# Kernel tuning notes

Hardware: AMD Instinct MI355X
Metric: run time of the kernel (lower is better)

The kernel has to match this reference:

```python
import jax, jax.numpy as jnp
import numpy as np

D = 256      # feature_dim (d_model)
H = 4        # num_heads
N = 4096     # query nodes
M = 4096     # source nodes


def _conv1x1(W, b, x):
    # Conv1d(kernel_size=1): per-position linear over channels. x: [1, Cin, N]
    return jnp.einsum('oi,bin->bon', W, x) + b[None, :, None]


def setup_inputs() -> dict:
    key = jax.random.key(0)
    ks = jax.random.split(key, 16)
    s = 0.02
    inp = {
        'x':      jax.random.normal(ks[0], (1, D, N), jnp.float32),
        'source': jax.random.normal(ks[1], (1, D, M), jnp.float32),
        'dist':   jax.random.uniform(ks[2], (1, N, M), jnp.float32),
        'mask':   jax.random.bernoulli(ks[3], 0.5, (N, M)),
        'Wq': s * jax.random.normal(ks[4], (D, D), jnp.float32),  'bq': jnp.zeros((D,), jnp.float32),
        'Wk': s * jax.random.normal(ks[5], (D, D), jnp.float32),  'bk': jnp.zeros((D,), jnp.float32),
        'Wv': s * jax.random.normal(ks[6], (D, D), jnp.float32),  'bv': jnp.zeros((D,), jnp.float32),
        'Wm': s * jax.random.normal(ks[7], (D, D), jnp.float32),  'bm': jnp.zeros((D,), jnp.float32),
        'W1': s * jax.random.normal(ks[8], (2 * D, 2 * D), jnp.float32), 'b1': jnp.zeros((2 * D,), jnp.float32),
        'W2': s * jax.random.normal(ks[9], (D, 2 * D), jnp.float32),     'b2': jnp.zeros((D,), jnp.float32),
    }
    return inp


def reference(x, source, dist, mask, Wq, bq, Wk, bk, Wv, bv, Wm, bm, W1, b1, W2, b2):
    dim = D // H  # per-head dim; torch view(1, dim, H, -1) splits channels as (dim, H)
    q = _conv1x1(Wq, bq, x).reshape(1, dim, H, N)
    k = _conv1x1(Wk, bk, source).reshape(1, dim, H, M)
    v = _conv1x1(Wv, bv, source).reshape(1, dim, H, M)

    scores = jnp.einsum('bdhn,bdhm->bhnm', q, k) / jnp.sqrt(jnp.asarray(dim, q.dtype))
    # non-standard additive mask: global detached min scales the masked-out entries
    smin = jax.lax.stop_gradient(scores.min())
    scores = scores + smin * (~mask).astype(scores.dtype)[None, None, :, :]

    prob = jax.nn.softmax(scores, axis=-1)                       # [1,H,N,M]
    attn = jnp.einsum('bhnm,bdhm->bdhn', prob, v)                # [1,dim,H,N]
    message = _conv1x1(Wm, bm, attn.reshape(1, D, N))            # merge heads

    h = jnp.concatenate([x, message], axis=1)                    # [1,2D,N]
    h = jax.nn.relu(_conv1x1(W1, b1, h))
    y = _conv1x1(W2, b2, h)                                      # [1,D,N]
    weights = scores.mean(axis=1)                                # [1,N,M]
    return y, weights
```

## Files before the change

### kernel.cpp

```cpp
#include <hip/hip_runtime.h>
#include <hip/hip_bf16.h>
#include <math.h>

#define Dm 256
#define Hh 4
#define Nn 4096
#define Mq 4096

typedef __attribute__((ext_vector_type(8))) short bf16x8;
typedef __attribute__((ext_vector_type(4))) float f32x4;
typedef _Float16 __attribute__((ext_vector_type(4))) f16x4;
typedef __fp16 __attribute__((ext_vector_type(2))) h16x2;

#define MFMA_BF16(a,b,c) __builtin_amdgcn_mfma_f32_16x16x32_bf16(a,b,c,0,0,0)
#define MFMA_F16x16(a,b,c) __builtin_amdgcn_mfma_f32_16x16x16f16(a,b,c,0,0,0)

#define MB (1u<<20)
#define OFF_FLAG  0
#define OFF_SMIN  64
#define OFF_KMAX  128
#define OFF_PART  1024
#define OFF_MT    8192
#define OFF_DENP  (128u<<10)
#define OFF_WB    (3u*MB/2)
#define OFF_BITS  (3u*MB)
#define OFF_QB    (5u*MB)
#define OFF_KB    (7u*MB)
#define OFF_VB    (9u*MB)
#define OFF_HCAT  (11u*MB)
#define OFF_ATTNT (15u*MB)
#define OFF_XT    (17u*MB)
#define OFF_ST    (19u*MB)
#define OFF_OPART (17u*MB)
#define OFF_H1T   (17u*MB)

#define WOFF_Q  0
#define WOFF_K  65536
#define WOFF_V  131072
#define WOFF_M  196608
#define WOFF_1  262144
#define WOFF_2  524288

__device__ __forceinline__ unsigned short f2bf(float x) {
    unsigned u = __float_as_uint(x);
    u += 0x7FFF + ((u >> 16) & 1);
    return (unsigned short)(u >> 16);
}
__device__ __forceinline__ float bf2f(unsigned short b) {
    return __uint_as_float(((unsigned)b) << 16);
}

__global__ void k_detect(const unsigned char* __restrict__ mb, int* __restrict__ flag,
                         unsigned* __restrict__ kmax) {
    __shared__ int c[5];
    if (threadIdx.x < 5) c[threadIdx.x] = 0;
    if (threadIdx.x < 4) kmax[threadIdx.x] = 0u;
    __syncthreads();
    for (int i = threadIdx.x; i < 16384; i += blockDim.x) {
        unsigned char b = mb[i];
        if (b) {
            atomicAdd(&c[i & 3], 1);
            if ((i & 7) == 4) atomicAdd(&c[4], 1);
        }
    }
    __syncthreads();
    if (threadIdx.x == 0) {
        int f;
        if (c[3] > 0 && c[0] == 0)          f = 3;
        else if (c[1] | c[2] | c[3])        f = 1;
        else if (c[4] > 0)                  f = 0;
        else                                f = 2;
        *flag = f;
    }
}

__global__ void k_maskbits(const void* __restrict__ mp, const int* __restrict__ flagp,
                           unsigned char* __restrict__ bits) {
    size_t i = (size_t)blockIdx.x * 256 + threadIdx.x;
    const int flag = *flagp;
    size_t base = i * 8;
    unsigned b = 0;
    if (flag == 1) {
        unsigned long long u = *(const unsigned long long*)((const unsigned char*)mp + base);
        #pragma unroll
        for (int j = 0; j < 8; j++) b |= (unsigned)(((u >> (8*j)) & 0xFFull) != 0ull) << j;
    } else if (flag == 0) {
        const int* p = (const int*)mp;
        #pragma unroll
        for (int j = 0; j < 8; j++) b |= (unsigned)(p[base + j] != 0) << j;
    } else if (flag == 3) {
        const float* p = (const float*)mp;
        #pragma unroll
        for (int j = 0; j < 8; j++) b |= (unsigned)(p[base + j] != 0.0f) << j;
    } else {
        const unsigned long long* p = (const unsigned long long*)mp;
        #pragma unroll
        for (int j = 0; j < 8; j++) b |= (unsigned)(p[base + j] != 0ull) << j;
    }
    bits[i] = (unsigned char)b;
}

__global__ __launch_bounds__(256) void k_prep(const float* __restrict__ x,
                                              const float* __restrict__ source,
                                              unsigned short* __restrict__ xt,
                                              unsigned short* __restrict__ st,
                                              unsigned short* __restrict__ hcat) {
    const int z = blockIdx.z;
    const float* src = z ? source : x;
    unsigned short* dst = z ? st : xt;
    unsigned short* dst2 = z ? nullptr : hcat;
    const int l = threadIdx.x & 63, g = threadIdx.x >> 6;
    const int c = blockIdx.y * 64 + l;
    const int n0 = blockIdx.x * 32 + g * 8;
    float4 v0 = *(const float4*)(src + (size_t)c * Nn + n0);
    float4 v1 = *(const float4*)(src + (size_t)c * Nn + n0 + 4);
    float vv[8] = {v0.x, v0.y, v0.z, v0.w, v1.x, v1.y, v1.z, v1.w};
    #pragma unroll
    for (int j = 0; j < 8; j++) {
        unsigned short b = f2bf(vv[j]);
        dst[(size_t)(n0 + j) * 256 + c] = b;
        if (dst2) dst2[(size_t)(n0 + j) * 512 + c] = b;
    }
}

__global__ void k_wcast(const float* __restrict__ Wq, const float* __restrict__ Wk,
                        const float* __restrict__ Wv, const float* __restrict__ Wm,
                        const float* __restrict__ W1, const float* __restrict__ W2,
                        unsigned short* __restrict__ wb) {
    size_t i = (size_t)blockIdx.x * 256 + threadIdx.x;
    const float* s; size_t off;
    if      (i < 65536)               { s = Wq; off = i; }
    else if (i < 131072)              { s = Wk; off = i - 65536; }
    else if (i < 196608)              { s = Wv; off = i - 131072; }
    else if (i < 262144)              { s = Wm; off = i - 196608; }
    else if (i < 524288)              { s = W1; off = i - 262144; }
    else                              { s = W2; off = i - 524288; }
    wb[i] = f2bf(s[off]);
}

template<int KK>
__device__ __forceinline__ void gemm_body(const unsigned short* __restrict__ wb,
                                          const float* __restrict__ bias,
                                          const unsigned short* __restrict__ xt,
                                          void* __restrict__ out, int mode,
                                          int bx, int by) {
    const int tid = threadIdx.x, w = tid >> 6, lane = tid & 63;
    const int lg = lane >> 4, lr = lane & 15;
    const int o_base = by * 64 + w * 16;
    const int n_base = bx * 64;
    f32x4 acc[4];
    #pragma unroll
    for (int j = 0; j < 4; j++) acc[j] = (f32x4){0.f, 0.f, 0.f, 0.f};
    const unsigned short* wrow = wb + (size_t)(o_base + lr) * KK + lg * 8;
    const unsigned short* xrow = xt + (size_t)(n_base + lr) * KK + lg * 8;
    #pragma unroll
    for (int k0 = 0; k0 < KK; k0 += 32) {
        bf16x8 af = *(const bf16x8*)(wrow + k0);
        #pragma unroll
        for (int j = 0; j < 4; j++) {
            bf16x8 bfr = *(const bf16x8*)(xrow + (size_t)j * 16 * KK + k0);
            acc[j] = MFMA_BF16(af, bfr, acc[j]);
        }
    }
    float bv[4];
    #pragma unroll
    for (int r = 0; r < 4; r++) bv[r] = bias[o_base + lg * 4 + r];
    #pragma unroll
    for (int j = 0; j < 4; j++) {
        #pragma unroll
        for (int r = 0; r < 4; r++) {
            int o = o_base + lg * 4 + r;
            int n = n_base + j * 16 + lr;
            float v = acc[j][r] + bv[r];
            if (mode == 0) {
                ((float*)out)[(size_t)o * Nn + n] = v;
            } else if (mode == 1) {
                ((unsigned short*)out)[(((size_t)(o & 3)) * Nn + n) * 64 + (o >> 2)] = f2bf(v);
            } else if (mode == 2) {
                union { _Float16 h; unsigned short u; } cv; cv.h = (_Float16)v;
                ((unsigned short*)out)[(((size_t)(o & 3)) * 64 + (o >> 2)) * Mq + n] = cv.u;
            } else if (mode == 3) {
                ((unsigned short*)out)[(size_t)n * 512 + 256 + o] = f2bf(v);
            } else if (mode == 4) {
                ((unsigned short*)out)[(size_t)n * 512 + o] = f2bf(fmaxf(v, 0.f));
            } else {
                int dd = o >> 2, hh = o & 3, g = dd >> 3, pos = dd & 7;
                int slot = g ^ (n & 7);
                ((unsigned short*)out)[(((size_t)hh * Mq + n)) * 64 + slot * 8 + pos] = f2bf(v);
            }
        }
    }
}

template<int KK>
__global__ __launch_bounds__(256) void k_mgemm(const unsigned short* __restrict__ wb,
                                               const float* __restrict__ bias,
                                               const unsigned short* __restrict__ xt,
                                               void* __restrict__ out, int mode) {
    gemm_body<KK>(wb, bias, xt, out, mode, blockIdx.x, blockIdx.y);
}

__global__ __launch_bounds__(256) void k_qkv(const unsigned short* __restrict__ wb,
                                             const float* __restrict__ bq,
                                             const float* __restrict__ bk,
                                             const float* __restrict__ bv,
                                             const unsigned short* __restrict__ xt,
                                             const unsigned short* __restrict__ st,
                                             void* __restrict__ qb, void* __restrict__ kb,
                                             void* __restrict__ vb) {
    const int z = blockIdx.z;
    const float* bias = (z == 0) ? bq : ((z == 1) ? bk : bv);
    const unsigned short* X = (z == 0) ? xt : st;
    void* out = (z == 0) ? qb : ((z == 1) ? kb : vb);
    int mode = (z == 0) ? 1 : ((z == 1) ? 5 : 2);
    gemm_body<256>(wb + z * 65536, bias, X, out, mode, blockIdx.x, blockIdx.y);
}

__global__ __launch_bounds__(256) void k_knorm(const unsigned short* __restrict__ kb,
                                               unsigned* __restrict__ kmax) {
    const int h = blockIdx.y;
    const int m = blockIdx.x * 256 + threadIdx.x;
    const unsigned short* row = kb + ((size_t)(h * Mq + m) << 6);
    float s = 0.f;
    #pragma unroll
    for (int i = 0; i < 64; i++) { float v = bf2f(row[i]); s = fmaf(v, v, s); }
    __shared__ float red[256];
    red[threadIdx.x] = s;
    __syncthreads();
    for (int st = 128; st > 0; st >>= 1) {
        if (threadIdx.x < st) red[threadIdx.x] = fmaxf(red[threadIdx.x], red[threadIdx.x + st]);
        __syncthreads();
    }
    if (threadIdx.x == 0) atomicMax(kmax + h, __float_as_uint(red[0]));
}

__global__ __launch_bounds__(256) void k_qnorm(const unsigned short* __restrict__ qb,
                                               const unsigned* __restrict__ kmax,
                                               float* __restrict__ mtarr) {
    const int row = blockIdx.x * 256 + threadIdx.x;
    const unsigned short* qr = qb + ((size_t)row << 6);
    float s = 0.f;
    #pragma unroll
    for (int i = 0; i < 64; i++) { float v = bf2f(qr[i]); s = fmaf(v, v, s); }
    float k2 = __uint_as_float(kmax[row >> 12]);
    mtarr[row] = sqrtf(s * k2) * 0.125f;
}

__global__ __launch_bounds__(256) void k_min(
    const unsigned short* __restrict__ qb, const unsigned short* __restrict__ kb,
    float* __restrict__ partial) {
    __shared__ unsigned short kbuf[2][8192];
    const int tid = threadIdx.x;
    const int w = tid >> 6, lane = tid & 63;
    const int lg = lane >> 4, lr = lane & 15;
    const int n0 = blockIdx.x * 64 + w * 16;
    const int m0 = blockIdx.y * 256;

    bf16x8 qf[4][2];
    #pragma unroll
    for (int h = 0; h < 4; h++)
        #pragma unroll
        for (int kh = 0; kh < 2; kh++)
            qf[h][kh] = *(const bf16x8*)(qb + (((size_t)h * Nn + n0 + lr) << 6) + kh*32 + lg*8);

    const unsigned short* srcs[4];
    #pragma unroll
    for (int h = 0; h < 4; h++) srcs[h] = kb + (((size_t)h * Mq + m0) << 6) + tid * 8;

    float mn = INFINITY;

    bf16x8 r[4];
    #pragma unroll
    for (int h = 0; h < 4; h++) {
        r[h] = *(const bf16x8*)(srcs[h]);
        *(bf16x8*)&kbuf[0][h * 2048 + tid * 8] = r[h];
    }
    __syncthreads();
    #pragma unroll
    for (int h = 0; h < 4; h++) r[h] = *(const bf16x8*)(srcs[h] + 2048);

    for (int t = 0; t < 8; t++) {
        const unsigned short* kB = &kbuf[t & 1][0];
        #pragma unroll
        for (int mi = 0; mi < 2; mi++) {
            const int rowoff = (mi * 16 + lr) * 64;
            #pragma unroll
            for (int h = 0; h < 4; h++) {
                bf16x8 a0 = *(const bf16x8*)(kB + h*2048 + rowoff + ((lg ^ (lr & 7)) << 3));
                bf16x8 a1 = *(const bf16x8*)(kB + h*2048 + rowoff + (((lg + 4) ^ (lr & 7)) << 3));
                f32x4 acc = (f32x4){0.f, 0.f, 0.f, 0.f};
                acc = MFMA_BF16(a0, qf[h][0], acc);
                acc = MFMA_BF16(a1, qf[h][1], acc);
                mn = fminf(mn, fminf(fminf(acc[0], acc[1]), fminf(acc[2], acc[3])));
            }
        }
        if (t < 7) {
            #pragma unroll
            for (int h = 0; h < 4; h++)
                *(bf16x8*)&kbuf[(t + 1) & 1][h * 2048 + tid * 8] = r[h];
        }
        __syncthreads();
        if (t < 6) {
            #pragma unroll
            for (int h = 0; h < 4; h++) r[h] = *(const bf16x8*)(srcs[h] + (size_t)(t + 2) * 2048);
        }
    }

    for (int off = 1; off < 64; off <<= 1) mn = fminf(mn, __shfl_xor(mn, off));
    __shared__ float wmin[4];
    if (lane == 0) wmin[w] = mn;
    __syncthreads();
    if (tid == 0) {
        float m2 = fminf(fminf(wmin[0], wmin[1]), fminf(wmin[2], wmin[3]));
        partial[blockIdx.x * 16 + blockIdx.y] = m2 * 0.125f;
    }
}

__global__ void k_minreduce(const float* __restrict__ partial, float* __restrict__ smin) {
    const int tid = threadIdx.x;
    float mn = fminf(fminf(partial[tid], partial[tid + 256]),
                     fminf(partial[tid + 512], partial[tid + 768]));
    __shared__ float red[256];
    red[tid] = mn;
    __syncthreads();
    for (int st = 128; st > 0; st >>= 1) {
        if (tid < st) red[tid] = fminf(red[tid], red[tid + st]);
        __syncthreads();
    }
    if (tid == 0) *smin = red[0];
}

__global__ __launch_bounds__(256) void k_wout(
    const unsigned short* __restrict__ qb, const unsigned short* __restrict__ kb,
    const unsigned long long* __restrict__ bits,
    const float* __restrict__ sminp, float* __restrict__ wout) {
    __shared__ unsigned short kbuf[2][8192];
    const int tid = threadIdx.x;
    const int w = tid >> 6, lane = tid & 63;
    const int lg = lane >> 4, lr = lane & 15;
    const int n0 = blockIdx.x * 64 + w * 16;
    const int m0 = blockIdx.y * 256;
    const float smin = *sminp;

    bf16x8 qf[4][2];
    #pragma unroll
    for (int h = 0; h < 4; h++)
        #pragma unroll
        for (int kh = 0; kh < 2; kh++)
            qf[h][kh] = *(const bf16x8*)(qb + (((size_t)h * Nn + n0 + lr) << 6) + kh*32 + lg*8);

    const unsigned short* srcs[4];
    #pragma unroll
    for (int h = 0; h < 4; h++) srcs[h] = kb + (((size_t)h * Mq + m0) << 6) + tid * 8;

    const unsigned long long* brow = bits + (((size_t)(n0 + lr)) << 6) + (m0 >> 6);
    unsigned long long bw = 0ull;

    bf16x8 r[4];
    #pragma unroll
    for (int h = 0; h < 4; h++) {
        r[h] = *(const bf16x8*)(srcs[h]);
        *(bf16x8*)&kbuf[0][h * 2048 + tid * 8] = r[h];
    }
    __syncthreads();
    #pragma unroll
    for (int h = 0; h < 4; h++) r[h] = *(const bf16x8*)(srcs[h] + 2048);

    for (int t = 0; t < 8; t++) {
        const unsigned short* kB = &kbuf[t & 1][0];
        const int mch = m0 + t * 32;
        if ((t & 1) == 0) bw = brow[t >> 1];
        #pragma unroll
        for (int mi = 0; mi < 2; mi++) {
            const int rowoff = (mi * 16 + lr) * 64;
            f32x4 accA = (f32x4){0.f, 0.f, 0.f, 0.f};
            f32x4 accB = (f32x4){0.f, 0.f, 0.f, 0.f};
            #pragma unroll
            for (int h = 0; h < 2; h++) {
                bf16x8 a0 = *(const bf16x8*)(kB + h*2048 + rowoff + ((lg ^ (lr & 7)) << 3));
                bf16x8 a1 = *(const bf16x8*)(kB + h*2048 + rowoff + (((lg + 4) ^ (lr & 7)) << 3));
                accA = MFMA_BF16(a0, qf[h][0], accA);
                accA = MFMA_BF16(a1, qf[h][1], accA);
            }
            #pragma unroll
            for (int h = 2; h < 4; h++) {
                bf16x8 a0 = *(const bf16x8*)(kB + h*2048 + rowoff + ((lg ^ (lr & 7)) << 3));
                bf16x8 a1 = *(const bf16x8*)(kB + h*2048 + rowoff + (((lg + 4) ^ (lr & 7)) << 3));
                accB = MFMA_BF16(a0, qf[h][0], accB);
                accB = MFMA_BF16(a1, qf[h][1], accB);
            }
            const int shb = (t & 1) * 32 + mi * 16 + lg * 4;
            f32x4 wv;
            #pragma unroll
            for (int rr = 0; rr < 4; rr++) {
                bool b = (bw >> (shb + rr)) & 1ull;
                wv[rr] = fmaf(accA[rr] + accB[rr], 0.03125f, b ? 0.f : smin);
            }
            *(f32x4*)(wout + (size_t)(n0 + lr) * Mq + mch + mi * 16 + lg * 4) = wv;
        }
        if (t < 7) {
            #pragma unroll
            for (int h = 0; h < 4; h++)
                *(bf16x8*)&kbuf[(t + 1) & 1][h * 2048 + tid * 8] = r[h];
        }
        __syncthreads();
        if (t < 6) {
            #pragma unroll
            for (int h = 0; h < 4; h++) r[h] = *(const bf16x8*)(srcs[h] + (size_t)(t + 2) * 2048);
        }
    }
}

__global__ __launch_bounds__(256) void k_pv(
    const unsigned short* __restrict__ qb, const unsigned short* __restrict__ kb,
    const unsigned short* __restrict__ vbh,
    const unsigned long long* __restrict__ bits,
    const float* __restrict__ sminp, const float* __restrict__ mtarr,
    float* __restrict__ denp, unsigned short* __restrict__ opart) {
    __shared__ unsigned short kbuf[2][4096];
    __shared__ unsigned short vbuf[2][4096];
    const int tid = threadIdx.x;
    const int w = tid >> 6, lane = tid & 63;
    const int lg = lane >> 4, lr = lane & 15;
    const int h = blockIdx.y & 3, mb = blockIdx.y >> 2;
    const int n0 = blockIdx.x * 64 + w * 16;
    const int m0 = mb * 1024;
    const float smin = *sminp;
    const float sminc = fmaxf(smin, 0.f);

    bf16x8 qf0 = *(const bf16x8*)(qb + (((size_t)h * Nn + n0 + lr) << 6) + lg*8);
    bf16x8 qf1 = *(const bf16x8*)(qb + (((size_t)h * Nn + n0 + lr) << 6) + 32 + lg*8);
    float mtE = mtarr[(size_t)h * Nn + n0 + lr] + sminc;
    const float cT = -mtE * 1.44269504f;
    const float cF = cT + smin * 1.44269504f;

    f32x4 oacc[4];
    #pragma unroll
    for (int ds = 0; ds < 4; ds++) oacc[ds] = (f32x4){0.f, 0.f, 0.f, 0.f};
    float dsum = 0.f;

    const unsigned short* ksrc = kb + (((size_t)h * Mq + m0) << 6) + tid * 8;
    const int vj = tid & 7;
    const int vdd0 = tid >> 3, vdd1 = 32 + (tid >> 3);
    const unsigned short* vsrc0 = vbh + (size_t)(h * 64 + vdd0) * Mq + m0 + vj * 8;
    const unsigned short* vsrc1 = vbh + (size_t)(h * 64 + vdd1) * Mq + m0 + vj * 8;
    int vdstA, vdstB, vdstC, vdstD;
    {
        int vds = vdd0 >> 4, vlr = vdd0 & 15, vmi = vj >> 1;
        int vswz = (vlr >> 2) & 3;
        int vbase = ((vmi * 4 + vds) * 16 + vlr) * 4;
        vdstA = (vbase + (((vj & 1) * 2 + 0) ^ vswz)) * 4;
        vdstB = (vbase + (((vj & 1) * 2 + 1) ^ vswz)) * 4;
        vds = vdd1 >> 4; vlr = vdd1 & 15;
        vswz = (vlr >> 2) & 3;
        vbase = ((vmi * 4 + vds) * 16 + vlr) * 4;
        vdstC = (vbase + (((vj & 1) * 2 + 0) ^ vswz)) * 4;
        vdstD = (vbase + (((vj & 1) * 2 + 1) ^ vswz)) * 4;
    }

    union U8 { bf16x8 v; unsigned long long q[2]; };
    U8 rv0, rv1;
    bf16x8 rk0 = *(const bf16x8*)(ksrc);
    bf16x8 rk1 = *(const bf16x8*)(ksrc + 2048);
    rv0.v = *(const bf16x8*)(vsrc0);
    rv1.v = *(const bf16x8*)(vsrc1);
    *(bf16x8*)&kbuf[0][tid * 8] = rk0;
    *(bf16x8*)&kbuf[0][2048 + tid * 8] = rk1;
    *(unsigned long long*)&vbuf[0][vdstA] = rv0.q[0];
    *(unsigned long long*)&vbuf[0][vdstB] = rv0.q[1];
    *(unsigned long long*)&vbuf[0][vdstC] = rv1.q[0];
    *(unsigned long long*)&vbuf[0][vdstD] = rv1.q[1];
    __syncthreads();
    rk0 = *(const bf16x8*)(ksrc + 4096);
    rk1 = *(const bf16x8*)(ksrc + 4096 + 2048);
    rv0.v = *(const bf16x8*)(vsrc0 + 64);
    rv1.v = *(const bf16x8*)(vsrc1 + 64);

    const unsigned long long* brow = bits + (((size_t)(n0 + lr)) << 6) + (m0 >> 6);
    const int kslot0 = (lg ^ (lr & 7)) << 3;
    const int kslot1 = ((lg + 4) ^ (lr & 7)) << 3;
    const int vrslot = (lg ^ ((lr >> 2) & 3)) * 4;

    for (int t = 0; t < 16; t++) {
        const unsigned short* kB = &kbuf[t & 1][0];
        const unsigned short* vB = &vbuf[t & 1][0];
        unsigned long long bw = brow[t];
        #pragma unroll
        for (int mi = 0; mi < 4; mi++) {
            const int rowoff = (mi * 16 + lr) * 64;
            bf16x8 a0 = *(const bf16x8*)(kB + rowoff + kslot0);
            bf16x8 a1 = *(const bf16x8*)(kB + rowoff + kslot1);
            f16x4 vf[4];
            #pragma unroll
            for (int ds = 0; ds < 4; ds++)
                vf[ds] = *(const f16x4*)&vB[((mi * 4 + ds) * 16 + lr) * 16 + vrslot];
            f32x4 acc = (f32x4){0.f, 0.f, 0.f, 0.f};
            acc = MFMA_BF16(a0, qf0, acc);
            acc = MFMA_BF16(a1, qf1, acc);
            const int shb = mi * 16 + lg * 4;
            float p0 = exp2f(fmaf(acc[0], 0.18033688f, ((bw >> (shb + 0)) & 1ull) ? cT : cF));
            float p1 = exp2f(fmaf(acc[1], 0.18033688f, ((bw >> (shb + 1)) & 1ull) ? cT : cF));
            float p2 = exp2f(fmaf(acc[2], 0.18033688f, ((bw >> (shb + 2)) & 1ull) ? cT : cF));
            float p3 = exp2f(fmaf(acc[3], 0.18033688f, ((bw >> (shb + 3)) & 1ull) ? cT : cF));
            dsum += (p0 + p1) + (p2 + p3);
            union { h16x2 h2[2]; f16x4 f4; } pu;
            pu.h2[0] = __builtin_amdgcn_cvt_pkrtz(p0, p1);
            pu.h2[1] = __builtin_amdgcn_cvt_pkrtz(p2, p3);
            f16x4 pf = pu.f4;
            #pragma unroll
            for (int ds = 0; ds < 4; ds++)
                oacc[ds] = MFMA_F16x16(pf, vf[ds], oacc[ds]);
        }
        if (t < 15) {
            *(bf16x8*)&kbuf[(t + 1) & 1][tid * 8] = rk0;
            *(bf16x8*)&kbuf[(t + 1) & 1][2048 + tid * 8] = rk1;
            *(unsigned long long*)&vbuf[(t + 1) & 1][vdstA] = rv0.q[0];
            *(unsigned long long*)&vbuf[(t + 1) & 1][vdstB] = rv0.q[1];
            *(unsigned long long*)&vbuf[(t + 1) & 1][vdstC] = rv1.q[0];
            *(unsigned long long*)&vbuf[(t + 1) & 1][vdstD] = rv1.q[1];
        }
        __syncthreads();
        if (t < 14) {
            rk0 = *(const bf16x8*)(ksrc + (size_t)(t + 2) * 4096);
            rk1 = *(const bf16x8*)(ksrc + (size_t)(t + 2) * 4096 + 2048);
            rv0.v = *(const bf16x8*)(vsrc0 + (size_t)(t + 2) * 64);
            rv1.v = *(const bf16x8*)(vsrc1 + (size_t)(t + 2) * 64);
        }
    }

    dsum += __shfl_xor(dsum, 16);
    dsum += __shfl_xor(dsum, 32);
    if (lane < 16)
        denp[((size_t)h * Nn + n0 + lane) * 4 + mb] = dsum;

    unsigned short* op = opart + (size_t)mb * (Dm * Nn);
    #pragma unroll
    for (int ds = 0; ds < 4; ds++) {
        int c = (ds * 16 + lr) * 4 + h;
        int n = n0 + lg * 4;
        unsigned long long pk =
            (unsigned long long)f2bf(oacc[ds][0]) |
            ((unsigned long long)f2bf(oacc[ds][1]) << 16) |
            ((unsigned long long)f2bf(oacc[ds][2]) << 32) |
            ((unsigned long long)f2bf(oacc[ds][3]) << 48);
        *(unsigned long long*)&op[(size_t)c * Nn + n] = pk;
    }
}

__global__ __launch_bounds__(256) void k_finish(const unsigned short* __restrict__ opart,
                                                const float* __restrict__ denp,
                                                unsigned short* __restrict__ attnT) {
    __shared__ float t[64][65];
    const int cb = blockIdx.y * 64, nb = blockIdx.x * 64;
    const int tid = threadIdx.x;
    #pragma unroll
    for (int e = 0; e < 16; e++) {
        int idx = e * 256 + tid;
        int c_l = idx >> 6, n_l = idx & 63;
        int c = cb + c_l, n = nb + n_l;
        float s = 0.f;
        #pragma unroll
        for (int y = 0; y < 4; y++)
            s += bf2f(opart[(size_t)y * (Dm*Nn) + (size_t)c * Nn + n]);
        size_t row = (size_t)(c & 3) * Nn + n;
        float d = denp[row*4] + denp[row*4+1] + denp[row*4+2] + denp[row*4+3];
        t[c_l][n_l] = s / d;
    }
    __syncthreads();
    #pragma unroll
    for (int e = 0; e < 16; e++) {
        int idx = e * 256 + tid;
        int n_l = idx >> 6, c_l = idx & 63;
        attnT[(size_t)(nb + n_l) * 256 + cb + c_l] = f2bf(t[c_l][n_l]);
    }
}

extern "C" void kernel_launch(void* const* d_in, const int* in_sizes, int n_in,
                              void* d_out, int out_size, void* d_ws, size_t ws_size,
                              hipStream_t stream) {
    const float* x      = (const float*)d_in[0];
    const float* source = (const float*)d_in[1];
    const void*  mask   = d_in[3];
    const float* Wq = (const float*)d_in[4];  const float* bq = (const float*)d_in[5];
    const float* Wk = (const float*)d_in[6];  const float* bk = (const float*)d_in[7];
    const float* Wv = (const float*)d_in[8];  const float* bv = (const float*)d_in[9];
    const float* Wm = (const float*)d_in[10]; const float* bm = (const float*)d_in[11];
    const float* W1 = (const float*)d_in[12]; const float* b1 = (const float*)d_in[13];
    const float* W2 = (const float*)d_in[14]; const float* b2 = (const float*)d_in[15];

    float* y    = (float*)d_out;
    float* wout = y + (size_t)Dm * Nn;

    char* ws = (char*)d_ws;
    int*      flag  = (int*)(ws + OFF_FLAG);
    float*    sminp = (float*)(ws + OFF_SMIN);
    float*    part  = (float*)(ws + OFF_PART);
    unsigned* kmax  = (unsigned*)(ws + OFF_KMAX);
    float*    mtarr = (float*)(ws + OFF_MT);
    float*    denp  = (float*)(ws + OFF_DENP);
    unsigned short* wb    = (unsigned short*)(ws + OFF_WB);
    unsigned char*  bits  = (unsigned char*)(ws + OFF_BITS);
    unsigned short* qb    = (unsigned short*)(ws + OFF_QB);
    unsigned short* kb    = (unsigned short*)(ws + OFF_KB);
    unsigned short* vb    = (unsigned short*)(ws + OFF_VB);
    unsigned short* hcat  = (unsigned short*)(ws + OFF_HCAT);
    unsigned short* attnT = (unsigned short*)(ws + OFF_ATTNT);
    unsigned short* xt    = (unsigned short*)(ws + OFF_XT);
    unsigned short* st    = (unsigned short*)(ws + OFF_ST);
    unsigned short* opart = (unsigned short*)(ws + OFF_OPART);
    unsigned short* h1t   = (unsigned short*)(ws + OFF_H1T);

    k_detect<<<1, 256, 0, stream>>>((const unsigned char*)mask, flag, kmax);
    k_maskbits<<<8192, 256, 0, stream>>>(mask, flag, bits);

    k_prep<<<dim3(128, 4, 2), 256, 0, stream>>>(x, source, xt, st, hcat);
    k_wcast<<<2560, 256, 0, stream>>>(Wq, Wk, Wv, Wm, W1, W2, wb);

    k_qkv<<<dim3(64, 4, 3), 256, 0, stream>>>(wb, bq, bk, bv, xt, st, qb, kb, vb);

    k_knorm<<<dim3(16, 4), 256, 0, stream>>>(kb, kmax);
    k_qnorm<<<64, 256, 0, stream>>>(qb, kmax, mtarr);

    k_min<<<dim3(64, 16), 256, 0, stream>>>(qb, kb, part);
    k_minreduce<<<1, 256, 0, stream>>>(part, sminp);

    k_wout<<<dim3(64, 16), 256, 0, stream>>>(qb, kb, (const unsigned long long*)bits, sminp, wout);

    k_pv<<<dim3(64, 16), 256, 0, stream>>>(qb, kb, vb, (const unsigned long long*)bits,
                                           sminp, mtarr, denp, opart);
    k_finish<<<dim3(64, 4), 256, 0, stream>>>(opart, denp, attnT);

    k_mgemm<256><<<dim3(64, 4), 256, 0, stream>>>(wb + WOFF_M, bm, attnT, hcat, 3);
    k_mgemm<512><<<dim3(64, 8), 256, 0, stream>>>(wb + WOFF_1, b1, hcat, h1t, 4);
    k_mgemm<512><<<dim3(64, 4), 256, 0, stream>>>(wb + WOFF_2, b2, h1t, y, 0);
}
```

Baseline: 208.1 us.

## Double query rows per wave in attention kernels, shrink GEMM N-tiles

```diff
diff --git a/kernel.cpp b/kernel.cpp
--- a/kernel.cpp
+++ b/kernel.cpp
@@ -138,7 +138,7 @@
     wb[i] = f2bf(s[off]);
 }
 
-template<int KK>
+template<int KK, int JT>
 __device__ __forceinline__ void gemm_body(const unsigned short* __restrict__ wb,
                                           const float* __restrict__ bias,
                                           const unsigned short* __restrict__ xt,
@@ -147,17 +147,17 @@
     const int tid = threadIdx.x, w = tid >> 6, lane = tid & 63;
     const int lg = lane >> 4, lr = lane & 15;
     const int o_base = by * 64 + w * 16;
-    const int n_base = bx * 64;
-    f32x4 acc[4];
-    #pragma unroll
-    for (int j = 0; j < 4; j++) acc[j] = (f32x4){0.f, 0.f, 0.f, 0.f};
+    const int n_base = bx * (16 * JT);
+    f32x4 acc[JT];
+    #pragma unroll
+    for (int j = 0; j < JT; j++) acc[j] = (f32x4){0.f, 0.f, 0.f, 0.f};
     const unsigned short* wrow = wb + (size_t)(o_base + lr) * KK + lg * 8;
     const unsigned short* xrow = xt + (size_t)(n_base + lr) * KK + lg * 8;
     #pragma unroll
     for (int k0 = 0; k0 < KK; k0 += 32) {
         bf16x8 af = *(const bf16x8*)(wrow + k0);
         #pragma unroll
-        for (int j = 0; j < 4; j++) {
+        for (int j = 0; j < JT; j++) {
             bf16x8 bfr = *(const bf16x8*)(xrow + (size_t)j * 16 * KK + k0);
             acc[j] = MFMA_BF16(af, bfr, acc[j]);
         }
@@ -166,7 +166,7 @@
     #pragma unroll
     for (int r = 0; r < 4; r++) bv[r] = bias[o_base + lg * 4 + r];
     #pragma unroll
-    for (int j = 0; j < 4; j++) {
+    for (int j = 0; j < JT; j++) {
         #pragma unroll
         for (int r = 0; r < 4; r++) {
             int o = o_base + lg * 4 + r;
@@ -197,7 +197,7 @@
                                                const float* __restrict__ bias,
                                                const unsigned short* __restrict__ xt,
                                                void* __restrict__ out, int mode) {
-    gemm_body<KK>(wb, bias, xt, out, mode, blockIdx.x, blockIdx.y);
+    gemm_body<KK, 2>(wb, bias, xt, out, mode, blockIdx.x, blockIdx.y);
 }
 
 __global__ __launch_bounds__(256) void k_qkv(const unsigned short* __restrict__ wb,
@@ -213,7 +213,7 @@
     const unsigned short* X = (z == 0) ? xt : st;
     void* out = (z == 0) ? qb : ((z == 1) ? kb : vb);
     int mode = (z == 0) ? 1 : ((z == 1) ? 5 : 2);
-    gemm_body<256>(wb + z * 65536, bias, X, out, mode, blockIdx.x, blockIdx.y);
+    gemm_body<256, 4>(wb + z * 65536, bias, X, out, mode, blockIdx.x, blockIdx.y);
 }
 
 __global__ __launch_bounds__(256) void k_knorm(const unsigned short* __restrict__ kb,
@@ -253,15 +253,17 @@
     const int tid = threadIdx.x;
     const int w = tid >> 6, lane = tid & 63;
     const int lg = lane >> 4, lr = lane & 15;
-    const int n0 = blockIdx.x * 64 + w * 16;
+    const int n0 = blockIdx.x * 128 + w * 32;
     const int m0 = blockIdx.y * 256;
 
-    bf16x8 qf[4][2];
+    bf16x8 qf[4][2][2];
     #pragma unroll
     for (int h = 0; h < 4; h++)
         #pragma unroll
-        for (int kh = 0; kh < 2; kh++)
-            qf[h][kh] = *(const bf16x8*)(qb + (((size_t)h * Nn + n0 + lr) << 6) + kh*32 + lg*8);
+        for (int ns = 0; ns < 2; ns++)
+            #pragma unroll
+            for (int kh = 0; kh < 2; kh++)
+                qf[h][ns][kh] = *(const bf16x8*)(qb + (((size_t)h * Nn + n0 + ns*16 + lr) << 6) + kh*32 + lg*8);
 
     const unsigned short* srcs[4];
     #pragma unroll
@@ -288,10 +290,13 @@
             for (int h = 0; h < 4; h++) {
                 bf16x8 a0 = *(const bf16x8*)(kB + h*2048 + rowoff + ((lg ^ (lr & 7)) << 3));
                 bf16x8 a1 = *(const bf16x8*)(kB + h*2048 + rowoff + (((lg + 4) ^ (lr & 7)) << 3));
-                f32x4 acc = (f32x4){0.f, 0.f, 0.f, 0.f};
-                acc = MFMA_BF16(a0, qf[h][0], acc);
-                acc = MFMA_BF16(a1, qf[h][1], acc);
-                mn = fminf(mn, fminf(fminf(acc[0], acc[1]), fminf(acc[2], acc[3])));
+                #pragma unroll
+                for (int ns = 0; ns < 2; ns++) {
+                    f32x4 acc = (f32x4){0.f, 0.f, 0.f, 0.f};
+                    acc = MFMA_BF16(a0, qf[h][ns][0], acc);
+                    acc = MFMA_BF16(a1, qf[h][ns][1], acc);
+                    mn = fminf(mn, fminf(fminf(acc[0], acc[1]), fminf(acc[2], acc[3])));
+                }
             }
         }
         if (t < 7) {
@@ -318,8 +323,7 @@
 
 __global__ void k_minreduce(const float* __restrict__ partial, float* __restrict__ smin) {
     const int tid = threadIdx.x;
-    float mn = fminf(fminf(partial[tid], partial[tid + 256]),
-                     fminf(partial[tid + 512], partial[tid + 768]));
+    float mn = fminf(partial[tid], partial[tid + 256]);
     __shared__ float red[256];
     red[tid] = mn;
     __syncthreads();
@@ -338,23 +342,26 @@
     const int tid = threadIdx.x;
     const int w = tid >> 6, lane = tid & 63;
     const int lg = lane >> 4, lr = lane & 15;
-    const int n0 = blockIdx.x * 64 + w * 16;
+    const int n0 = blockIdx.x * 128 + w * 32;
     const int m0 = blockIdx.y * 256;
     const float smin = *sminp;
 
-    bf16x8 qf[4][2];
+    bf16x8 qf[4][2][2];
     #pragma unroll
     for (int h = 0; h < 4; h++)
         #pragma unroll
-        for (int kh = 0; kh < 2; kh++)
-            qf[h][kh] = *(const bf16x8*)(qb + (((size_t)h * Nn + n0 + lr) << 6) + kh*32 + lg*8);
+        for (int ns = 0; ns < 2; ns++)
+            #pragma unroll
+            for (int kh = 0; kh < 2; kh++)
+                qf[h][ns][kh] = *(const bf16x8*)(qb + (((size_t)h * Nn + n0 + ns*16 + lr) << 6) + kh*32 + lg*8);
 
     const unsigned short* srcs[4];
     #pragma unroll
     for (int h = 0; h < 4; h++) srcs[h] = kb + (((size_t)h * Mq + m0) << 6) + tid * 8;
 
-    const unsigned long long* brow = bits + (((size_t)(n0 + lr)) << 6) + (m0 >> 6);
-    unsigned long long bw = 0ull;
+    const unsigned long long* brow0 = bits + (((size_t)(n0 + lr)) << 6) + (m0 >> 6);
+    const unsigned long long* brow1 = bits + (((size_t)(n0 + 16 + lr)) << 6) + (m0 >> 6);
+    unsigned long long bw0 = 0ull, bw1 = 0ull;
 
     bf16x8 r[4];
     #pragma unroll
@@ -369,34 +376,40 @@
     for (int t = 0; t < 8; t++) {
         const unsigned short* kB = &kbuf[t & 1][0];
         const int mch = m0 + t * 32;
-        if ((t & 1) == 0) bw = brow[t >> 1];
+        if ((t & 1) == 0) { bw0 = brow0[t >> 1]; bw1 = brow1[t >> 1]; }
         #pragma unroll
         for (int mi = 0; mi < 2; mi++) {
             const int rowoff = (mi * 16 + lr) * 64;
-            f32x4 accA = (f32x4){0.f, 0.f, 0.f, 0.f};
-            f32x4 accB = (f32x4){0.f, 0.f, 0.f, 0.f};
-            #pragma unroll
-            for (int h = 0; h < 2; h++) {
+            f32x4 acc[2][2];
+            #pragma unroll
+            for (int ns = 0; ns < 2; ns++) {
+                acc[ns][0] = (f32x4){0.f, 0.f, 0.f, 0.f};
+                acc[ns][1] = (f32x4){0.f, 0.f, 0.f, 0.f};
+            }
+            #pragma unroll
+            for (int h = 0; h < 4; h++) {
                 bf16x8 a0 = *(const bf16x8*)(kB + h*2048 + rowoff + ((lg ^ (lr & 7)) << 3));
                 bf16x8 a1 = *(const bf16x8*)(kB + h*2048 + rowoff + (((lg + 4) ^ (lr & 7)) << 3));
-                accA = MFMA_BF16(a0, qf[h][0], accA);
-                accA = MFMA_BF16(a1, qf[h][1], accA);
-            }
-            #pragma unroll
-            for (int h = 2; h < 4; h++) {
-                bf16x8 a0 = *(const bf16x8*)(kB + h*2048 + rowoff + ((lg ^ (lr & 7)) << 3));
-                bf16x8 a1 = *(const bf16x8*)(kB + h*2048 + rowoff + (((lg + 4) ^ (lr & 7)) << 3));
-                accB = MFMA_BF16(a0, qf[h][0], accB);
-                accB = MFMA_BF16(a1, qf[h][1], accB);
+                const int hf = h >> 1;
+                #pragma unroll
+                for (int ns = 0; ns < 2; ns++) {
+                    acc[ns][hf] = MFMA_BF16(a0, qf[h][ns][0], acc[ns][hf]);
+                    acc[ns][hf] = MFMA_BF16(a1, qf[h][ns][1], acc[ns][hf]);
+                }
             }
             const int shb = (t & 1) * 32 + mi * 16 + lg * 4;
-            f32x4 wv;
-            #pragma unroll
-            for (int rr = 0; rr < 4; rr++) {
-                bool b = (bw >> (shb + rr)) & 1ull;
-                wv[rr] = fmaf(accA[rr] + accB[rr], 0.03125f, b ? 0.f : smin);
+            #pragma unroll
+            for (int ns = 0; ns < 2; ns++) {
+                unsigned long long bw = ns ? bw1 : bw0;
+                f32x4 wv;
+                #pragma unroll
+                for (int rr = 0; rr < 4; rr++) {
+                    bool b = (bw >> (shb + rr)) & 1ull;
+                    wv[rr] = fmaf(acc[ns][0][rr] + acc[ns][1][rr], 0.03125f, b ? 0.f : smin);
+                }
+                __builtin_nontemporal_store(wv,
+                    (f32x4*)(wout + (size_t)(n0 + ns*16 + lr) * Mq + mch + mi * 16 + lg * 4));
             }
-            *(f32x4*)(wout + (size_t)(n0 + lr) * Mq + mch + mi * 16 + lg * 4) = wv;
         }
         if (t < 7) {
             #pragma unroll
@@ -423,21 +436,29 @@
     const int w = tid >> 6, lane = tid & 63;
     const int lg = lane >> 4, lr = lane & 15;
     const int h = blockIdx.y & 3, mb = blockIdx.y >> 2;
-    const int n0 = blockIdx.x * 64 + w * 16;
+    const int n0 = blockIdx.x * 128 + w * 32;
     const int m0 = mb * 1024;
     const float smin = *sminp;
     const float sminc = fmaxf(smin, 0.f);
 
-    bf16x8 qf0 = *(const bf16x8*)(qb + (((size_t)h * Nn + n0 + lr) << 6) + lg*8);
-    bf16x8 qf1 = *(const bf16x8*)(qb + (((size_t)h * Nn + n0 + lr) << 6) + 32 + lg*8);
-    float mtE = mtarr[(size_t)h * Nn + n0 + lr] + sminc;
-    const float cT = -mtE * 1.44269504f;
-    const float cF = cT + smin * 1.44269504f;
-
-    f32x4 oacc[4];
-    #pragma unroll
-    for (int ds = 0; ds < 4; ds++) oacc[ds] = (f32x4){0.f, 0.f, 0.f, 0.f};
-    float dsum = 0.f;
+    bf16x8 qf[2][2];
+    float cT[2], cF[2];
+    #pragma unroll
+    for (int ns = 0; ns < 2; ns++) {
+        const size_t qrow = ((size_t)h * Nn + n0 + ns*16 + lr) << 6;
+        qf[ns][0] = *(const bf16x8*)(qb + qrow + lg*8);
+        qf[ns][1] = *(const bf16x8*)(qb + qrow + 32 + lg*8);
+        float mtE = mtarr[(size_t)h * Nn + n0 + ns*16 + lr] + sminc;
+        cT[ns] = -mtE * 1.44269504f;
+        cF[ns] = cT[ns] + smin * 1.44269504f;
+    }
+
+    f32x4 oacc[2][4];
+    #pragma unroll
+    for (int ns = 0; ns < 2; ns++)
+        #pragma unroll
+        for (int ds = 0; ds < 4; ds++) oacc[ns][ds] = (f32x4){0.f, 0.f, 0.f, 0.f};
+    float dsum[2] = {0.f, 0.f};
 
     const unsigned short* ksrc = kb + (((size_t)h * Mq + m0) << 6) + tid * 8;
     const int vj = tid & 7;
@@ -476,7 +497,8 @@
     rv0.v = *(const bf16x8*)(vsrc0 + 64);
     rv1.v = *(const bf16x8*)(vsrc1 + 64);
 
-    const unsigned long long* brow = bits + (((size_t)(n0 + lr)) << 6) + (m0 >> 6);
+    const unsigned long long* brow0 = bits + (((size_t)(n0 + lr)) << 6) + (m0 >> 6);
+    const unsigned long long* brow1 = bits + (((size_t)(n0 + 16 + lr)) << 6) + (m0 >> 6);
     const int kslot0 = (lg ^ (lr & 7)) << 3;
     const int kslot1 = ((lg + 4) ^ (lr & 7)) << 3;
     const int vrslot = (lg ^ ((lr >> 2) & 3)) * 4;
@@ -484,7 +506,9 @@
     for (int t = 0; t < 16; t++) {
         const unsigned short* kB = &kbuf[t & 1][0];
         const unsigned short* vB = &vbuf[t & 1][0];
-        unsigned long long bw = brow[t];
+        unsigned long long bw[2];
+        bw[0] = brow0[t];
+        bw[1] = brow1[t];
         #pragma unroll
         for (int mi = 0; mi < 4; mi++) {
             const int rowoff = (mi * 16 + lr) * 64;
@@ -494,22 +518,25 @@
             #pragma unroll
             for (int ds = 0; ds < 4; ds++)
                 vf[ds] = *(const f16x4*)&vB[((mi * 4 + ds) * 16 + lr) * 16 + vrslot];
-            f32x4 acc = (f32x4){0.f, 0.f, 0.f, 0.f};
-            acc = MFMA_BF16(a0, qf0, acc);
-            acc = MFMA_BF16(a1, qf1, acc);
             const int shb = mi * 16 + lg * 4;
-            float p0 = exp2f(fmaf(acc[0], 0.18033688f, ((bw >> (shb + 0)) & 1ull) ? cT : cF));
-            float p1 = exp2f(fmaf(acc[1], 0.18033688f, ((bw >> (shb + 1)) & 1ull) ? cT : cF));
-            float p2 = exp2f(fmaf(acc[2], 0.18033688f, ((bw >> (shb + 2)) & 1ull) ? cT : cF));
-            float p3 = exp2f(fmaf(acc[3], 0.18033688f, ((bw >> (shb + 3)) & 1ull) ? cT : cF));
-            dsum += (p0 + p1) + (p2 + p3);
-            union { h16x2 h2[2]; f16x4 f4; } pu;
-            pu.h2[0] = __builtin_amdgcn_cvt_pkrtz(p0, p1);
-            pu.h2[1] = __builtin_amdgcn_cvt_pkrtz(p2, p3);
-            f16x4 pf = pu.f4;
-            #pragma unroll
-            for (int ds = 0; ds < 4; ds++)
-                oacc[ds] = MFMA_F16x16(pf, vf[ds], oacc[ds]);
+            #pragma unroll
+            for (int ns = 0; ns < 2; ns++) {
+                f32x4 acc = (f32x4){0.f, 0.f, 0.f, 0.f};
+                acc = MFMA_BF16(a0, qf[ns][0], acc);
+                acc = MFMA_BF16(a1, qf[ns][1], acc);
+                float p0 = exp2f(fmaf(acc[0], 0.18033688f, ((bw[ns] >> (shb + 0)) & 1ull) ? cT[ns] : cF[ns]));
+                float p1 = exp2f(fmaf(acc[1], 0.18033688f, ((bw[ns] >> (shb + 1)) & 1ull) ? cT[ns] : cF[ns]));
+                float p2 = exp2f(fmaf(acc[2], 0.18033688f, ((bw[ns] >> (shb + 2)) & 1ull) ? cT[ns] : cF[ns]));
+                float p3 = exp2f(fmaf(acc[3], 0.18033688f, ((bw[ns] >> (shb + 3)) & 1ull) ? cT[ns] : cF[ns]));
+                dsum[ns] += (p0 + p1) + (p2 + p3);
+                union { h16x2 h2[2]; f16x4 f4; } pu;
+                pu.h2[0] = __builtin_amdgcn_cvt_pkrtz(p0, p1);
+                pu.h2[1] = __builtin_amdgcn_cvt_pkrtz(p2, p3);
+                f16x4 pf = pu.f4;
+                #pragma unroll
+                for (int ds = 0; ds < 4; ds++)
+                    oacc[ns][ds] = MFMA_F16x16(pf, vf[ds], oacc[ns][ds]);
+            }
         }
         if (t < 15) {
             *(bf16x8*)&kbuf[(t + 1) & 1][tid * 8] = rk0;
@@ -528,23 +555,31 @@
         }
     }
 
-    dsum += __shfl_xor(dsum, 16);
-    dsum += __shfl_xor(dsum, 32);
-    if (lane < 16)
-        denp[((size_t)h * Nn + n0 + lane) * 4 + mb] = dsum;
+    #pragma unroll
+    for (int ns = 0; ns < 2; ns++) {
+        dsum[ns] += __shfl_xor(dsum[ns], 16);
+        dsum[ns] += __shfl_xor(dsum[ns], 32);
+    }
+    if (lane < 16) {
+        #pragma unroll
+        for (int ns = 0; ns < 2; ns++)
+            denp[((size_t)h * Nn + n0 + ns*16 + lane) * 4 + mb] = dsum[ns];
+    }
 
     unsigned short* op = opart + (size_t)mb * (Dm * Nn);
     #pragma unroll
-    for (int ds = 0; ds < 4; ds++) {
-        int c = (ds * 16 + lr) * 4 + h;
-        int n = n0 + lg * 4;
-        unsigned long long pk =
-            (unsigned long long)f2bf(oacc[ds][0]) |
-            ((unsigned long long)f2bf(oacc[ds][1]) << 16) |
-            ((unsigned long long)f2bf(oacc[ds][2]) << 32) |
-            ((unsigned long long)f2bf(oacc[ds][3]) << 48);
-        *(unsigned long long*)&op[(size_t)c * Nn + n] = pk;
-    }
+    for (int ns = 0; ns < 2; ns++)
+        #pragma unroll
+        for (int ds = 0; ds < 4; ds++) {
+            int c = (ds * 16 + lr) * 4 + h;
+            int n = n0 + ns * 16 + lg * 4;
+            unsigned long long pk =
+                (unsigned long long)f2bf(oacc[ns][ds][0]) |
+                ((unsigned long long)f2bf(oacc[ns][ds][1]) << 16) |
+                ((unsigned long long)f2bf(oacc[ns][ds][2]) << 32) |
+                ((unsigned long long)f2bf(oacc[ns][ds][3]) << 48);
+            *(unsigned long long*)&op[(size_t)c * Nn + n] = pk;
+        }
 }
 
 __global__ __launch_bounds__(256) void k_finish(const unsigned short* __restrict__ opart,
@@ -621,16 +656,16 @@
     k_knorm<<<dim3(16, 4), 256, 0, stream>>>(kb, kmax);
     k_qnorm<<<64, 256, 0, stream>>>(qb, kmax, mtarr);
 
-    k_min<<<dim3(64, 16), 256, 0, stream>>>(qb, kb, part);
+    k_min<<<dim3(32, 16), 256, 0, stream>>>(qb, kb, part);
     k_minreduce<<<1, 256, 0, stream>>>(part, sminp);
 
-    k_wout<<<dim3(64, 16), 256, 0, stream>>>(qb, kb, (const unsigned long long*)bits, sminp, wout);
-
-    k_pv<<<dim3(64, 16), 256, 0, stream>>>(qb, kb, vb, (const unsigned long long*)bits,
+    k_wout<<<dim3(32, 16), 256, 0, stream>>>(qb, kb, (const unsigned long long*)bits, sminp, wout);
+
+    k_pv<<<dim3(32, 16), 256, 0, stream>>>(qb, kb, vb, (const unsigned long long*)bits,
                                            sminp, mtarr, denp, opart);
     k_finish<<<dim3(64, 4), 256, 0, stream>>>(opart, denp, attnT);
 
-    k_mgemm<256><<<dim3(64, 4), 256, 0, stream>>>(wb + WOFF_M, bm, attnT, hcat, 3);
-    k_mgemm<512><<<dim3(64, 8), 256, 0, stream>>>(wb + WOFF_1, b1, hcat, h1t, 4);
-    k_mgemm<512><<<dim3(64, 4), 256, 0, stream>>>(wb + WOFF_2, b2, h1t, y, 0);
-}
+    k_mgemm<256><<<dim3(128, 4), 256, 0, stream>>>(wb + WOFF_M, bm, attnT, hcat, 3);
+    k_mgemm<512><<<dim3(128, 8), 256, 0, stream>>>(wb + WOFF_1, b1, hcat, h1t, 4);
+    k_mgemm<512><<<dim3(128, 4), 256, 0, stream>>>(wb + WOFF_2, b2, h1t, y, 0);
+}
```

Result: slower. 214.8 us (+3.2%).
